# Kernel optimization log

Hardware: AMD Instinct MI355X
Metric: run time of the kernel (lower is better)

Reference implementation:

```python
import jax, jax.numpy as jnp
import numpy as np

N = 100000
E = 1600000
IN_C, HID, HEADS, OUT_C = 128, 32, 4, 32
NEG_SLOPE = 0.2


def gat_layer(x, edge_index, W, att_src, att_dst, bias, concat):
    """PyG-style GATConv: h = xW, per-edge attention, segment softmax over dst, scatter-add."""
    n = x.shape[0]
    H, C = att_src.shape
    h = (x @ W).reshape(n, H, C)                      # [N, H, C]
    src, dst = edge_index[0], edge_index[1]
    a_s = jnp.sum(h * att_src, axis=-1)               # [N, H]
    a_d = jnp.sum(h * att_dst, axis=-1)               # [N, H]
    e = jax.nn.leaky_relu(a_s[src] + a_d[dst], NEG_SLOPE)   # [E, H]
    # numerically stable segment softmax over incoming edges of each dst node
    m = jax.ops.segment_max(e, dst, num_segments=n)   # [N, H]
    ex = jnp.exp(e - m[dst])
    denom = jax.ops.segment_sum(ex, dst, num_segments=n)
    alpha = ex / denom[dst]                           # [E, H]
    msg = h[src] * alpha[:, :, None]                  # [E, H, C]
    out = jax.ops.segment_sum(msg, dst, num_segments=n)  # [N, H, C]
    out = out.reshape(n, H * C) if concat else out.mean(axis=1)
    return out + bias


def add_self_loops(edge_index, n):
    ar = jnp.arange(n, dtype=edge_index.dtype)
    loops = jnp.stack([ar, ar])
    return jnp.concatenate([edge_index, loops], axis=1)


def setup_inputs() -> dict:
    key = jax.random.key(0)
    ks = jax.random.split(key, 10)
    x = jax.random.normal(ks[0], (N, IN_C), dtype=jnp.float32)
    edge_index = jax.random.randint(ks[1], (2, E), 0, N, dtype=jnp.int64)
    s = 0.1
    W1 = jax.random.normal(ks[2], (IN_C, HEADS * HID), dtype=jnp.float32) * s
    att_src1 = jax.random.normal(ks[3], (HEADS, HID), dtype=jnp.float32) * s
    att_dst1 = jax.random.normal(ks[4], (HEADS, HID), dtype=jnp.float32) * s
    b1 = jnp.zeros((HEADS * HID,), dtype=jnp.float32)
    W2 = jax.random.normal(ks[5], (HEADS * HID, OUT_C), dtype=jnp.float32) * s
    att_src2 = jax.random.normal(ks[6], (1, OUT_C), dtype=jnp.float32) * s
    att_dst2 = jax.random.normal(ks[7], (1, OUT_C), dtype=jnp.float32) * s
    b2 = jnp.zeros((OUT_C,), dtype=jnp.float32)
    return {"x": x, "edge_index": edge_index,
            "W1": W1, "att_src1": att_src1, "att_dst1": att_dst1, "b1": b1,
            "W2": W2, "att_src2": att_src2, "att_dst2": att_dst2, "b2": b2}


def reference(x, edge_index, W1, att_src1, att_dst1, b1, W2, att_src2, att_dst2, b2):
    ei = add_self_loops(edge_index, x.shape[0])
    h = gat_layer(x, ei, W1, att_src1, att_dst1, b1, concat=True)
    h = jax.nn.elu(h)
    h = gat_layer(h, ei, W2, att_src2, att_dst2, b2, concat=False)
    return jax.nn.log_softmax(h, axis=1)
```

## Files before the change

### kernel.cpp

```cpp
#include <hip/hip_runtime.h>
#include <hip/hip_fp16.h>
#include <math.h>

#define IN_C   128
#define HEADS  4
#define F1     128
#define OUT_C  32
#define NEG    0.2f
#define SH     8
#define CHA    8192
#define SCB    4096

__device__ __forceinline__ unsigned short f2h(float f) {
    return __half_as_ushort(__float2half_rn(f));
}
__device__ __forceinline__ float h2f(unsigned short u) {
    return __half2float(__ushort_as_half(u));
}
__device__ __forceinline__ float hlo(unsigned u) { return h2f((unsigned short)(u & 0xffffu)); }
__device__ __forceinline__ float hhi(unsigned u) { return h2f((unsigned short)(u >> 16)); }
__device__ __forceinline__ unsigned pk2(float a, float b) {
    return (unsigned)f2h(a) | ((unsigned)f2h(b) << 16);
}
typedef _Float16 h2v __attribute__((ext_vector_type(2)));
__device__ __forceinline__ h2v u2h2(unsigned u) {
    h2v r; __builtin_memcpy(&r, &u, 4); return r;
}
__device__ __forceinline__ float dot2(unsigned a, unsigned b, float c) {
    return __builtin_amdgcn_fdot2(u2h2(a), u2h2(b), c, false);
}
#define PERM_LO 0x05040100u
#define PERM_HI 0x07060302u
__device__ __forceinline__ float pdot(unsigned b, unsigned a, unsigned sel, h2v pv, float c) {
    return __builtin_amdgcn_fdot2(u2h2(__builtin_amdgcn_perm(b, a, sel)), pv, c, false);
}

__global__ __launch_bounds__(256) void k_bhist(
    const int* __restrict__ ei, int* __restrict__ bmat, int E_, int n, int NB, int NC)
{
    __shared__ int h[512];
    int t = threadIdx.x, c = blockIdx.x;
    for (int i = t; i < NB; i += 256) h[i] = 0;
    __syncthreads();
    int e0 = c * CHA, e1 = min(e0 + CHA, E_ + n);
    for (int e = e0 + t; e < e1; e += 256) {
        int d = (e < E_) ? ei[E_ + e] : e - E_;
        atomicAdd(&h[d >> SH], 1);
    }
    __syncthreads();
    for (int i = t; i < NB; i += 256) bmat[i * NC + c] = h[i];
}

__global__ __launch_bounds__(256) void k_scanA(
    int* __restrict__ bmat, int* __restrict__ bsums, int M)
{
    __shared__ int sm[256];
    int t = threadIdx.x;
    int base = blockIdx.x * SCB + t * 16;
    int v[16];
    int s = 0;
    #pragma unroll
    for (int j = 0; j < 16; ++j) {
        int i = base + j;
        v[j] = (i < M) ? bmat[i] : 0;
        s += v[j];
    }
    sm[t] = s;
    __syncthreads();
    for (int off = 1; off < 256; off <<= 1) {
        int a = (t >= off) ? sm[t - off] : 0;
        __syncthreads();
        sm[t] += a;
        __syncthreads();
    }
    int excl = sm[t] - s;
    #pragma unroll
    for (int j = 0; j < 16; ++j) {
        int i = base + j;
        if (i < M) bmat[i] = excl;
        excl += v[j];
    }
    if (t == 255) bsums[blockIdx.x] = sm[255];
}

__global__ __launch_bounds__(256) void k_scanB(int* __restrict__ bsums, int NBLK)
{
    __shared__ int sm[256];
    int t = threadIdx.x;
    int v = (t < NBLK) ? bsums[t] : 0;
    sm[t] = v;
    __syncthreads();
    for (int off = 1; off < 256; off <<= 1) {
        int a = (t >= off) ? sm[t - off] : 0;
        __syncthreads();
        sm[t] += a;
        __syncthreads();
    }
    if (t < NBLK) bsums[t] = sm[t] - v;
}


__global__ __launch_bounds__(256) void k_bscatter(
    const int* __restrict__ ei, const int* __restrict__ bmat,
    const int* __restrict__ bsums, unsigned* __restrict__ recs,
    int E_, int n, int NB, int NC)
{
    __shared__ int cur[512];
    int t = threadIdx.x, c = blockIdx.x;
    for (int i = t; i < NB; i += 256) {
        int m = i * NC + c;
        cur[i] = bmat[m] + bsums[m >> 12];
    }
    __syncthreads();
    int e0 = c * CHA, e1 = min(e0 + CHA, E_ + n);
    for (int e = e0 + t; e < e1; e += 256) {
        int s, d;
        if (e < E_) { s = ei[e]; d = ei[E_ + e]; } else { s = d = e - E_; }
        int b = d >> SH;
        int p = atomicAdd(&cur[b], 1);
        recs[p] = ((unsigned)(d & ((1 << SH) - 1)) << 17) | (unsigned)s;
    }
}

__global__ __launch_bounds__(256) void k_bfill(
    const unsigned* __restrict__ recs, const int* __restrict__ bmat,
    const int* __restrict__ bsums, int* __restrict__ row_off,
    int* __restrict__ csr, int n, int NB, int NC, int EE)
{
    __shared__ int deg[256];
    __shared__ int cur[256];
    int t = threadIdx.x, b = blockIdx.x;
    int m0 = b * NC;
    int r0 = bmat[m0] + bsums[m0 >> 12];
    int r1 = EE;
    if (b + 1 < NB) {
        int m1 = (b + 1) * NC;
        r1 = bmat[m1] + bsums[m1 >> 12];
    }
    deg[t] = 0;
    __syncthreads();
    for (int i = r0 + t; i < r1; i += 256)
        atomicAdd(&deg[recs[i] >> 17], 1);
    __syncthreads();
    int v = deg[t];
    for (int off = 1; off < 256; off <<= 1) {
        int a = (t >= off) ? deg[t - off] : 0;
        __syncthreads();
        deg[t] += a;
        __syncthreads();
    }
    int excl = deg[t] - v;
    int dst = (b << SH) + t;
    if (dst < n) row_off[dst] = r0 + excl;
    cur[t] = excl;
    if (b == NB - 1 && t == 0) row_off[n] = EE;
    __syncthreads();
    for (int i = r0 + t; i < r1; i += 256) {
        unsigned rec = recs[i];
        int dl = rec >> 17;
        int p = atomicAdd(&cur[dl], 1);
        csr[r0 + p] = (int)(rec & 0x1FFFFu);
    }
}

__global__ __launch_bounds__(256) void k_gemm1(
    const float* __restrict__ x, const float* __restrict__ W,
    const float* __restrict__ as_w, const float* __restrict__ ad_w,
    unsigned short* __restrict__ h1h, float* __restrict__ as1,
    float* __restrict__ ad1, int n)
{
    __shared__ unsigned Ws2[64 * 64];
    __shared__ unsigned xs2[64 * 64];
    int t = threadIdx.x;
    int half = blockIdx.x & 1;
    int n0 = (blockIdx.x >> 1) * 64;

    for (int i = t; i < 64 * 16; i += 256) {
        int k2 = i >> 4, c4 = (i & 15) * 4;
        const float* w0 = &W[(2 * k2) * 128 + half * 64 + c4];
        const float* w1 = &W[(2 * k2 + 1) * 128 + half * 64 + c4];
        float4 a = *(const float4*)w0;
        float4 b = *(const float4*)w1;
        uint4 p;
        p.x = pk2(a.x, b.x); p.y = pk2(a.y, b.y);
        p.z = pk2(a.z, b.z); p.w = pk2(a.w, b.w);
        *(uint4*)&Ws2[k2 * 64 + c4] = p;
    }
    for (int i = t; i < 64 * 32; i += 256) {
        int nl = i & 63, k4 = (i >> 6) * 4;
        int nn = n0 + nl;
        float4 v = (nn < n) ? *(const float4*)&x[(size_t)nn * 128 + k4]
                            : make_float4(0.f, 0.f, 0.f, 0.f);
        xs2[(k4 >> 1) * 64 + nl]       = pk2(v.x, v.y);
        xs2[((k4 >> 1) + 1) * 64 + nl] = pk2(v.z, v.w);
    }
    __syncthreads();

    int tx = t & 15, ty = t >> 4;
    float acc[4][4] = {};
    #pragma unroll 4
    for (int k2 = 0; k2 < 64; ++k2) {
        uint4 a = *(uint4*)&xs2[k2 * 64 + ty * 4];
        uint4 b = *(uint4*)&Ws2[k2 * 64 + tx * 4];
        unsigned av[4] = {a.x, a.y, a.z, a.w};
        unsigned bv[4] = {b.x, b.y, b.z, b.w};
        #pragma unroll
        for (int i = 0; i < 4; ++i)
            #pragma unroll
            for (int j = 0; j < 4; ++j)
                acc[i][j] = dot2(av[i], bv[j], acc[i][j]);
    }
    int cbase = half * 64 + tx * 4;
    float4 aws = *(const float4*)&as_w[cbase];
    float4 awd = *(const float4*)&ad_w[cbase];
    float sa[4], sd[4];
    #pragma unroll
    for (int i = 0; i < 4; ++i) {
        int nn = n0 + ty * 4 + i;
        sa[i] = acc[i][0]*aws.x + acc[i][1]*aws.y + acc[i][2]*aws.z + acc[i][3]*aws.w;
        sd[i] = acc[i][0]*awd.x + acc[i][1]*awd.y + acc[i][2]*awd.z + acc[i][3]*awd.w;
        if (nn < n) {
            ushort4 p;
            p.x = f2h(acc[i][0]); p.y = f2h(acc[i][1]);
            p.z = f2h(acc[i][2]); p.w = f2h(acc[i][3]);
            *(ushort4*)&h1h[(size_t)nn * 128 + cbase] = p;
        }
    }
    #pragma unroll
    for (int o = 1; o < 8; o <<= 1) {
        #pragma unroll
        for (int i = 0; i < 4; ++i) {
            sa[i] += __shfl_xor(sa[i], o);
            sd[i] += __shfl_xor(sd[i], o);
        }
    }
    if ((tx & 7) == 0) {
        int head = half * 2 + (tx >> 3);
        #pragma unroll
        for (int i = 0; i < 4; ++i) {
            int nn = n0 + ty * 4 + i;
            if (nn < n) {
                as1[(size_t)nn * 4 + head] = sa[i];
                ad1[(size_t)nn * 4 + head] = sd[i];
            }
        }
    }
}

__global__ __launch_bounds__(256) void k_gat1(
    const int* __restrict__ row_off, const int* __restrict__ csr,
    const float* __restrict__ as1, const float* __restrict__ ad1,
    const unsigned short* __restrict__ h1h, const float* __restrict__ b1,
    const float* __restrict__ W2, const float* __restrict__ as2w,
    const float* __restrict__ ad2w, unsigned short* __restrict__ h2h,
    float* __restrict__ as2, float* __restrict__ ad2, int n)
{
    __shared__ int      s_src[16][36];
    __shared__ unsigned s_pw[16][4][17];
    __shared__ unsigned W2s[64 * 32];
    __shared__ unsigned zs[16][66];
    int t = threadIdx.x;

    for (int i = t; i < 64 * 8; i += 256) {
        int k2 = i >> 3, c4 = (i & 7) * 4;
        float4 a = *(const float4*)&W2[(2 * k2) * 32 + c4];
        float4 b = *(const float4*)&W2[(2 * k2 + 1) * 32 + c4];
        uint4 p;
        p.x = pk2(a.x, b.x); p.y = pk2(a.y, b.y);
        p.z = pk2(a.z, b.z); p.w = pk2(a.w, b.w);
        *(uint4*)&W2s[k2 * 32 + c4] = p;
    }
    __syncthreads();

    int nb = t >> 4;
    int hl = t & 15;
    int node = blockIdx.x * 16 + nb;
    if (node < n) {
        int* ssrc = s_src[nb];
        unsigned (*spw)[17] = s_pw[nb];

        const char* h1b = (const char*)h1h;
        int chb  = hl << 4;
        int head = hl >> 2;

        float4 addv = *(const float4*)&ad1[(size_t)node * 4];
        int beg = row_off[node], end = row_off[node + 1];

        float sr0 = 0.f, sr1 = 0.f, sr2 = 0.f, sr3 = 0.f;
        float acc0 = 0.f, acc1 = 0.f, acc2 = 0.f, acc3 = 0.f;
        float acc4 = 0.f, acc5 = 0.f, acc6 = 0.f, acc7 = 0.f;

        for (int c = beg; c < end; c += 32) {
            int cnt = min(32, end - c);
            int e0 = hl << 1;
            float ls0 = 0.f, ls1 = 0.f, ls2 = 0.f, ls3 = 0.f;
            if (e0 < cnt) {
                int sA = csr[c + e0];
                ssrc[e0] = sA << 8;
                float4 avA = *(const float4*)(as1 + ((unsigned)sA << 2));
                float v;
                unsigned short qa0, qa1, qa2, qa3;
                unsigned short qb0 = 0, qb1 = 0, qb2 = 0, qb3 = 0;
                v = avA.x + addv.x; v = v > 0.f ? v : NEG * v; qa0 = f2h(__expf(fminf(v, 10.f)));
                v = avA.y + addv.y; v = v > 0.f ? v : NEG * v; qa1 = f2h(__expf(fminf(v, 10.f)));
                v = avA.z + addv.z; v = v > 0.f ? v : NEG * v; qa2 = f2h(__expf(fminf(v, 10.f)));
                v = avA.w + addv.w; v = v > 0.f ? v : NEG * v; qa3 = f2h(__expf(fminf(v, 10.f)));
                if (e0 + 1 < cnt) {
                    int sB = csr[c + e0 + 1];
                    ssrc[e0 + 1] = sB << 8;
                    float4 avB = *(const float4*)(as1 + ((unsigned)sB << 2));
                    v = avB.x + addv.x; v = v > 0.f ? v : NEG * v; qb0 = f2h(__expf(fminf(v, 10.f)));
                    v = avB.y + addv.y; v = v > 0.f ? v : NEG * v; qb1 = f2h(__expf(fminf(v, 10.f)));
                    v = avB.z + addv.z; v = v > 0.f ? v : NEG * v; qb2 = f2h(__expf(fminf(v, 10.f)));
                    v = avB.w + addv.w; v = v > 0.f ? v : NEG * v; qb3 = f2h(__expf(fminf(v, 10.f)));
                }
                spw[0][hl] = (unsigned)qa0 | ((unsigned)qb0 << 16);
                spw[1][hl] = (unsigned)qa1 | ((unsigned)qb1 << 16);
                spw[2][hl] = (unsigned)qa2 | ((unsigned)qb2 << 16);
                spw[3][hl] = (unsigned)qa3 | ((unsigned)qb3 << 16);
                ls0 = h2f(qa0) + h2f(qb0);
                ls1 = h2f(qa1) + h2f(qb1);
                ls2 = h2f(qa2) + h2f(qb2);
                ls3 = h2f(qa3) + h2f(qb3);
            }
            #pragma unroll
            for (int o = 8; o; o >>= 1) {
                ls0 += __shfl_xor(ls0, o);
                ls1 += __shfl_xor(ls1, o);
                ls2 += __shfl_xor(ls2, o);
                ls3 += __shfl_xor(ls3, o);
            }
            sr0 += ls0; sr1 += ls1; sr2 += ls2; sr3 += ls3;
            __threadfence_block();

            #define MAC8(A, B, pw) {                                          \
                h2v pv = u2h2(pw);                                            \
                acc0 = pdot(B.x, A.x, PERM_LO, pv, acc0);                     \
                acc1 = pdot(B.x, A.x, PERM_HI, pv, acc1);                     \
                acc2 = pdot(B.y, A.y, PERM_LO, pv, acc2);                     \
// ... 51 lines not shown
        }
        float srh = head == 0 ? sr0 : head == 1 ? sr1 : head == 2 ? sr2 : sr3;
        float inv = 1.0f / srh;
        float4 bb0 = *(const float4*)&b1[hl * 8];
        float4 bb1 = *(const float4*)&b1[hl * 8 + 4];
        float v0 = acc0 * inv + bb0.x;
        float v1 = acc1 * inv + bb0.y;
        float v2 = acc2 * inv + bb0.z;
        float v3 = acc3 * inv + bb0.w;
        float v4 = acc4 * inv + bb1.x;
        float v5 = acc5 * inv + bb1.y;
        float v6 = acc6 * inv + bb1.z;
        float v7 = acc7 * inv + bb1.w;
        v0 = v0 > 0.f ? v0 : (__expf(v0) - 1.f);
        v1 = v1 > 0.f ? v1 : (__expf(v1) - 1.f);
        v2 = v2 > 0.f ? v2 : (__expf(v2) - 1.f);
        v3 = v3 > 0.f ? v3 : (__expf(v3) - 1.f);
        v4 = v4 > 0.f ? v4 : (__expf(v4) - 1.f);
        v5 = v5 > 0.f ? v5 : (__expf(v5) - 1.f);
        v6 = v6 > 0.f ? v6 : (__expf(v6) - 1.f);
        v7 = v7 > 0.f ? v7 : (__expf(v7) - 1.f);

        unsigned* zrow = zs[nb];
        zrow[hl * 4 + 0] = pk2(v0, v1);
        zrow[hl * 4 + 1] = pk2(v2, v3);
        zrow[hl * 4 + 2] = pk2(v4, v5);
        zrow[hl * 4 + 3] = pk2(v6, v7);
        __threadfence_block();
        int c0 = hl * 2;
        float a0 = 0.f, a1 = 0.f;
        #pragma unroll 8
        for (int k2 = 0; k2 < 64; ++k2) {
            unsigned zp = zrow[k2];
            uint2 wp = *(const uint2*)&W2s[k2 * 32 + c0];
            a0 = dot2(zp, wp.x, a0);
            a1 = dot2(zp, wp.y, a1);
        }
        *(unsigned*)&h2h[(size_t)node * 32 + c0] = pk2(a0, a1);
        float2 asw = *(const float2*)&as2w[c0];
        float2 adw = *(const float2*)&ad2w[c0];
        float sa = a0 * asw.x + a1 * asw.y;
        float sd = a0 * adw.x + a1 * adw.y;
        #pragma unroll
        for (int o = 8; o; o >>= 1) {
            sa += __shfl_xor(sa, o);
            sd += __shfl_xor(sd, o);
        }
        if (hl == 0) { as2[node] = sa; ad2[node] = sd; }
    }
}

__global__ __launch_bounds__(256) void k_gat2(
    const int* __restrict__ row_off, const int* __restrict__ csr,
    const float* __restrict__ as2, const float* __restrict__ ad2,
    const unsigned short* __restrict__ h2h, const float* __restrict__ b2,
    float* __restrict__ y, int n)
{
    int nb = threadIdx.x >> 2;
    int hl = threadIdx.x & 3;
    int node = blockIdx.x * 64 + nb;
    if (node >= n) return;
    __shared__ int            s_src[64][34];
    __shared__ unsigned short s_p16[64][34];
    int* ssrc = s_src[nb];
    unsigned short* sp16 = s_p16[nb];

    const char* h2b = (const char*)h2h;
    int chb = hl << 4;

    float addv = ad2[node];
    int beg = row_off[node], end = row_off[node + 1];
    float sr = 0.f;
    float acc0 = 0.f, acc1 = 0.f, acc2 = 0.f, acc3 = 0.f;
    float acc4 = 0.f, acc5 = 0.f, acc6 = 0.f, acc7 = 0.f;

    for (int c = beg; c < end; c += 32) {
        int cnt = min(32, end - c);
        int e0 = hl << 3;
        float ls = 0.f;
        #pragma unroll
        for (int k = 0; k < 8; k += 2) {
            int e = e0 + k;
            if (e < cnt) {
                unsigned short qa, qb = 0;
                int sA = csr[c + e];
                ssrc[e] = sA << 6;
                float v = as2[(unsigned)sA] + addv;
                v = v > 0.f ? v : NEG * v;
                qa = f2h(__expf(fminf(v, 10.f)));
                if (e + 1 < cnt) {
                    int sB = csr[c + e + 1];
                    ssrc[e + 1] = sB << 6;
                    float w2 = as2[(unsigned)sB] + addv;
                    w2 = w2 > 0.f ? w2 : NEG * w2;
                    qb = f2h(__expf(fminf(w2, 10.f)));
                }
                *(unsigned*)&sp16[e] = (unsigned)qa | ((unsigned)qb << 16);
                ls += h2f(qa) + h2f(qb);
            }
        }
        ls += __shfl_xor(ls, 1);
        ls += __shfl_xor(ls, 2);
        sr += ls;
        __threadfence_block();

        #define PAIR2(j) {                                                    \
            int2 oo = *(const int2*)&ssrc[j];                                 \
            unsigned pp = *(const unsigned*)&sp16[j];                         \
            uint4 A = *(const uint4*)(h2b + (unsigned)(oo.x + chb));          \
            uint4 B = *(const uint4*)(h2b + (unsigned)(oo.y + chb));          \
            h2v pv = u2h2(pp);                                                \
            acc0 = pdot(B.x, A.x, PERM_LO, pv, acc0);                         \
            acc1 = pdot(B.x, A.x, PERM_HI, pv, acc1);                         \
            acc2 = pdot(B.y, A.y, PERM_LO, pv, acc2);                         \
            acc3 = pdot(B.y, A.y, PERM_HI, pv, acc3);                         \
            acc4 = pdot(B.z, A.z, PERM_LO, pv, acc4);                         \
            acc5 = pdot(B.z, A.z, PERM_HI, pv, acc5);                         \
            acc6 = pdot(B.w, A.w, PERM_LO, pv, acc6);                         \
            acc7 = pdot(B.w, A.w, PERM_HI, pv, acc7);                         \
        }
        int jj = 0;
        for (; jj + 4 <= cnt; jj += 4) {
            PAIR2(jj);
            PAIR2(jj + 2);
        }
        if (jj + 2 <= cnt) {
            PAIR2(jj);
            jj += 2;
        }
        if (jj < cnt) {
            int o0 = ssrc[jj];
            float p = h2f(sp16[jj]);
            uint4 A = *(const uint4*)(h2b + (unsigned)(o0 + chb));
            acc0 = fmaf(p, hlo(A.x), acc0);
            acc1 = fmaf(p, hhi(A.x), acc1);
            acc2 = fmaf(p, hlo(A.y), acc2);
            acc3 = fmaf(p, hhi(A.y), acc3);
            acc4 = fmaf(p, hlo(A.z), acc4);
            acc5 = fmaf(p, hhi(A.z), acc5);
            acc6 = fmaf(p, hlo(A.w), acc6);
            acc7 = fmaf(p, hhi(A.w), acc7);
        }
        #undef PAIR2
    }
    float inv = 1.0f / sr;
    float4 bb0 = *(const float4*)&b2[hl * 8];
    float4 bb1 = *(const float4*)&b2[hl * 8 + 4];
    float v0 = acc0 * inv + bb0.x;
    float v1 = acc1 * inv + bb0.y;
    float v2 = acc2 * inv + bb0.z;
    float v3 = acc3 * inv + bb0.w;
    float v4 = acc4 * inv + bb1.x;
    float v5 = acc5 * inv + bb1.y;
    float v6 = acc6 * inv + bb1.z;
    float v7 = acc7 * inv + bb1.w;
    float m = fmaxf(fmaxf(fmaxf(v0, v1), fmaxf(v2, v3)),
                    fmaxf(fmaxf(v4, v5), fmaxf(v6, v7)));
    m = fmaxf(m, __shfl_xor(m, 1));
    m = fmaxf(m, __shfl_xor(m, 2));
    float ss = __expf(v0 - m) + __expf(v1 - m) + __expf(v2 - m) + __expf(v3 - m)
             + __expf(v4 - m) + __expf(v5 - m) + __expf(v6 - m) + __expf(v7 - m);
    ss += __shfl_xor(ss, 1);
    ss += __shfl_xor(ss, 2);
    float lg = m + logf(ss);
    float* yr = &y[(size_t)node * OUT_C + hl * 8];
    *(float4*)yr       = make_float4(v0 - lg, v1 - lg, v2 - lg, v3 - lg);
    *(float4*)(yr + 4) = make_float4(v4 - lg, v5 - lg, v6 - lg, v7 - lg);
}

extern "C" void kernel_launch(void* const* d_in, const int* in_sizes, int n_in,
                              void* d_out, int out_size, void* d_ws, size_t ws_size,
                              hipStream_t stream) {
    const float* x    = (const float*)d_in[0];
    const int*   ei   = (const int*)d_in[1];
    const float* W1   = (const float*)d_in[2];
    const float* as1w = (const float*)d_in[3];
    const float* ad1w = (const float*)d_in[4];
    const float* b1   = (const float*)d_in[5];
    const float* W2   = (const float*)d_in[6];
    const float* as2w = (const float*)d_in[7];
    const float* ad2w = (const float*)d_in[8];
    const float* b2   = (const float*)d_in[9];
    float* out = (float*)d_out;

    int n  = in_sizes[0] / IN_C;
    int E_ = in_sizes[1] / 2;
    int EE = E_ + n;

    int NB = (n + (1 << SH) - 1) >> SH;
    int NC = (EE + CHA - 1) / CHA;
    int M  = NB * NC;
    int NBLK = (M + SCB - 1) / SCB;

    char* w = (char*)d_ws;
    size_t off = 0;
    auto take = [&](size_t elems) { void* p = w + off; off += ((elems * 4 + 255) & ~(size_t)255); return p; };
    int* bmat      = (int*)take((size_t)M);
    int* bsums     = (int*)take(256);
    unsigned* recs = (unsigned*)take((size_t)EE);
    int* row_off   = (int*)take((size_t)n + 1);
    int* csr       = (int*)take((size_t)EE);
    float* as1     = (float*)take((size_t)n * 4);
    float* ad1     = (float*)take((size_t)n * 4);
    unsigned short* h1h = (unsigned short*)take((size_t)n * 64);
    unsigned short* h2h = (unsigned short*)take((size_t)n * 16);
    float* as2     = (float*)take((size_t)n);
    float* ad2     = (float*)take((size_t)n);

    k_bhist   <<<NC, 256, 0, stream>>>(ei, bmat, E_, n, NB, NC);
    k_scanA   <<<NBLK, 256, 0, stream>>>(bmat, bsums, M);
    k_scanB   <<<1, 256, 0, stream>>>(bsums, NBLK);
    k_bscatter<<<NC, 256, 0, stream>>>(ei, bmat, bsums, recs, E_, n, NB, NC);
    k_bfill   <<<NB, 256, 0, stream>>>(recs, bmat, bsums, row_off, csr, n, NB, NC, EE);

    int nt = (n + 63) / 64;
    k_gemm1<<<nt * 2, 256, 0, stream>>>(x, W1, as1w, ad1w, h1h, as1, ad1, n);

    int gG = (n + 15) / 16;
    k_gat1<<<gG, 256, 0, stream>>>(row_off, csr, as1, ad1, h1h, b1,
                                   W2, as2w, ad2w, h2h, as2, ad2, n);

    int gG2 = (n + 63) / 64;
    k_gat2<<<gG2, 256, 0, stream>>>(row_off, csr, as2, ad2, h2h, b2, out, n);
}
```

Measured before the change: 302.2 us.

## Fuse histogram into MFMA-based layer-1 GEMM and fold block-sum scan into consumers

Replaces the dot2-based layer-1 GEMM with an MFMA 16x16x32 f16 kernel. It uses swizzled LDS tiles and one block per 64 nodes covering all 128 columns, and adds an LDS-transposed coalesced store of h1. The destination-bucket histogram blocks are merged into the same launch as extra blocks, so the two independent jobs run concurrently. The single-block scanB kernel is removed, and each consumer recomputes the tiny bsums prefix with a warp scan. This cuts kernel launches and speeds up the GEMM. In exchange, every block reserves 48KB of LDS, which may lower occupancy for the histogram blocks, and the write-back relies on a block-level fence rather than a barrier.

Measured after the change: 300.4 us. About the same (-0.6%).

```diff
diff --git a/kernel.cpp b/kernel.cpp
--- a/kernel.cpp
+++ b/kernel.cpp
@@ -22,7 +22,10 @@
 __device__ __forceinline__ unsigned pk2(float a, float b) {
     return (unsigned)f2h(a) | ((unsigned)f2h(b) << 16);
 }
-typedef _Float16 h2v __attribute__((ext_vector_type(2)));
+typedef _Float16 h2v  __attribute__((ext_vector_type(2)));
+typedef _Float16 f16x4v __attribute__((ext_vector_type(4)));
+typedef _Float16 f16x8v __attribute__((ext_vector_type(8)));
+typedef float    f32x4v __attribute__((ext_vector_type(4)));
 __device__ __forceinline__ h2v u2h2(unsigned u) {
     h2v r; __builtin_memcpy(&r, &u, 4); return r;
 }
@@ -35,20 +38,121 @@
     return __builtin_amdgcn_fdot2(u2h2(__builtin_amdgcn_perm(b, a, sel)), pv, c, false);
 }
 
-__global__ __launch_bounds__(256) void k_bhist(
-    const int* __restrict__ ei, int* __restrict__ bmat, int E_, int n, int NB, int NC)
+__global__ __launch_bounds__(256) void k_gemm1h(
+    const float* __restrict__ x, const float* __restrict__ W,
+    const float* __restrict__ as_w, const float* __restrict__ ad_w,
+    const int* __restrict__ ei, int* __restrict__ bmat,
+    unsigned short* __restrict__ h1h, float* __restrict__ as1,
+    float* __restrict__ ad1, int n, int E_, int NB, int NC)
 {
-    __shared__ int h[512];
-    int t = threadIdx.x, c = blockIdx.x;
-    for (int i = t; i < NB; i += 256) h[i] = 0;
-    __syncthreads();
-    int e0 = c * CHA, e1 = min(e0 + CHA, E_ + n);
-    for (int e = e0 + t; e < e1; e += 256) {
-        int d = (e < E_) ? ei[E_ + e] : e - E_;
-        atomicAdd(&h[d >> SH], 1);
-    }
-    __syncthreads();
-    for (int i = t; i < NB; i += 256) bmat[i * NC + c] = h[i];
+    __shared__ char lds[49152];
+    int t = threadIdx.x;
+
+    if ((int)blockIdx.x < NC) {
+        int* h = (int*)lds;
+        int c = blockIdx.x;
+        for (int i = t; i < NB; i += 256) h[i] = 0;
+        __syncthreads();
+        int e0 = c * CHA, e1 = min(e0 + CHA, E_ + n);
+        for (int e = e0 + t; e < e1; e += 256) {
+            int d = (e < E_) ? ei[E_ + e] : e - E_;
+            atomicAdd(&h[d >> SH], 1);
+        }
+        __syncthreads();
+        for (int i = t; i < NB; i += 256) bmat[i * NC + c] = h[i];
+        return;
+    }
+
+    char* xhB = lds;
+    char* wtB = lds + 16384;
+    int n0 = ((int)blockIdx.x - NC) * 64;
+
+    for (int i = t; i < 128 * 32; i += 256) {
+        int k = i >> 5, c4 = (i & 31) * 4;
+        float4 wv = *(const float4*)&W[k * 128 + c4];
+        float vv[4] = {wv.x, wv.y, wv.z, wv.w};
+        #pragma unroll
+        for (int j = 0; j < 4; ++j) {
+            int cc = c4 + j;
+            *(_Float16*)(wtB + cc * 256 + ((2 * k) ^ ((cc & 7) << 4))) = (_Float16)vv[j];
+        }
+    }
+    for (int i = t; i < 64 * 32; i += 256) {
+        int node = i >> 5, k4 = (i & 31) * 4;
+        int nn = n0 + node;
+        float4 v = (nn < n) ? *(const float4*)&x[(size_t)nn * 128 + k4]
+                            : make_float4(0.f, 0.f, 0.f, 0.f);
+        f16x4v hv = { (_Float16)v.x, (_Float16)v.y, (_Float16)v.z, (_Float16)v.w };
+        *(f16x4v*)(xhB + node * 256 + ((2 * k4) ^ ((node & 7) << 4))) = hv;
+    }
+    __syncthreads();
+
+    int w = t >> 6, l = t & 63, g = l >> 4, cl = l & 15;
+    int arow = w * 16 + cl;
+    f32x4v acc[8] = {};
+    #pragma unroll
+    for (int s = 0; s < 4; ++s) {
+        int k2 = 2 * (s * 32 + g * 8);
+        f16x8v a = *(f16x8v*)(xhB + arow * 256 + (k2 ^ ((arow & 7) << 4)));
+        #pragma unroll
+        for (int tt = 0; tt < 8; ++tt) {
+            int col = tt * 16 + cl;
+            f16x8v b = *(f16x8v*)(wtB + col * 256 + (k2 ^ ((col & 7) << 4)));
+            acc[tt] = __builtin_amdgcn_mfma_f32_16x16x32_f16(a, b, acc[tt], 0, 0, 0);
+        }
+    }
+
+    #pragma unroll
+    for (int h = 0; h < 4; ++h) {
+        float asw0 = as_w[h * 32 + cl],      adw0 = ad_w[h * 32 + cl];
+        float asw1 = as_w[h * 32 + 16 + cl], adw1 = ad_w[h * 32 + 16 + cl];
+        float ps[4], pd[4];
+        #pragma unroll
+        for (int r = 0; r < 4; ++r) {
+            ps[r] = acc[2 * h][r] * asw0 + acc[2 * h + 1][r] * asw1;
+            pd[r] = acc[2 * h][r] * adw0 + acc[2 * h + 1][r] * adw1;
+        }
+        #pragma unroll
+        for (int o = 1; o < 16; o <<= 1) {
+            #pragma unroll
+            for (int r = 0; r < 4; ++r) {
+                ps[r] += __shfl_xor(ps[r], o);
+                pd[r] += __shfl_xor(pd[r], o);
+            }
+        }
+        if (cl == h) {
+            #pragma unroll
+            for (int r = 0; r < 4; ++r) {
+                int node = n0 + w * 16 + g * 4 + r;
+                if (node < n) {
+                    as1[(size_t)node * 4 + h] = ps[r];
+                    ad1[(size_t)node * 4 + h] = pd[r];
+                }
+            }
+        }
+    }
+
+    #pragma unroll
+    for (int tt = 0; tt < 8; ++tt) {
+        int cc = tt * 16 + cl;
+        #pragma unroll
+        for (int r = 0; r < 4; ++r) {
+            int rl = w * 16 + g * 4 + r;
+            *(_Float16*)(xhB + rl * 256 + ((2 * cc) ^ ((rl & 7) << 4))) = (_Float16)acc[tt][r];
+        }
+    }
+    __threadfence_block();
+    int rl = w * 16 + cl;
+    int node = n0 + rl;
+    if (node < n) {
+        #pragma unroll
+        for (int i = 0; i < 4; ++i) {
+            int slot = g * 4 + i;
+            uint4 val = *(uint4*)(xhB + rl * 256 + slot * 16);
+            int c0 = 8 * (slot ^ (rl & 7));
+            *(uint4*)&h1h[(size_t)node * 128 + c0] = val;
+        }
+    }
 }
 
 __global__ __launch_bounds__(256) void k_scanA(
@@ -83,33 +187,29 @@
     if (t == 255) bsums[blockIdx.x] = sm[255];
 }
 
-__global__ __launch_bounds__(256) void k_scanB(int* __restrict__ bsums, int NBLK)
-{
-    __shared__ int sm[256];
-    int t = threadIdx.x;
-    int v = (t < NBLK) ? bsums[t] : 0;
-    sm[t] = v;
-    __syncthreads();
-    for (int off = 1; off < 256; off <<= 1) {
-        int a = (t >= off) ? sm[t - off] : 0;
-        __syncthreads();
-        sm[t] += a;
-        __syncthreads();
-    }
-    if (t < NBLK) bsums[t] = sm[t] - v;
-}
-
 
 __global__ __launch_bounds__(256) void k_bscatter(
     const int* __restrict__ ei, const int* __restrict__ bmat,
     const int* __restrict__ bsums, unsigned* __restrict__ recs,
-    int E_, int n, int NB, int NC)
+    int E_, int n, int NB, int NC, int NBLK)
 {
     __shared__ int cur[512];
+    __shared__ int pref[32];
     int t = threadIdx.x, c = blockIdx.x;
+    if (t < 32) {
+        int v0 = (t < NBLK) ? bsums[t] : 0;
+        int v = v0;
+        #pragma unroll
+        for (int o = 1; o < 32; o <<= 1) {
+            int u = __shfl_up(v, o);
+            if (t >= o) v += u;
+        }
+        pref[t] = v - v0;
+    }
+    __syncthreads();
     for (int i = t; i < NB; i += 256) {
         int m = i * NC + c;
-        cur[i] = bmat[m] + bsums[m >> 12];
+        cur[i] = bmat[m] + pref[m >> 12];
     }
     __syncthreads();
     int e0 = c * CHA, e1 = min(e0 + CHA, E_ + n);
@@ -125,20 +225,31 @@
 __global__ __launch_bounds__(256) void k_bfill(
     const unsigned* __restrict__ recs, const int* __restrict__ bmat,
     const int* __restrict__ bsums, int* __restrict__ row_off,
-    int* __restrict__ csr, int n, int NB, int NC, int EE)
+    int* __restrict__ csr, int n, int NB, int NC, int EE, int NBLK)
 {
     __shared__ int deg[256];
     __shared__ int cur[256];
+    __shared__ int pref[32];
     int t = threadIdx.x, b = blockIdx.x;
+    if (t < 32) {
+        int v0 = (t < NBLK) ? bsums[t] : 0;
+        int v = v0;
+        #pragma unroll
+        for (int o = 1; o < 32; o <<= 1) {
+            int u = __shfl_up(v, o);
+            if (t >= o) v += u;
+        }
+        pref[t] = v - v0;
+    }
+    deg[t] = 0;
+    __syncthreads();
     int m0 = b * NC;
-    int r0 = bmat[m0] + bsums[m0 >> 12];
+    int r0 = bmat[m0] + pref[m0 >> 12];
     int r1 = EE;
     if (b + 1 < NB) {
         int m1 = (b + 1) * NC;
-        r1 = bmat[m1] + bsums[m1 >> 12];
-    }
-    deg[t] = 0;
-    __syncthreads();
+        r1 = bmat[m1] + pref[m1 >> 12];
+    }
     for (int i = r0 + t; i < r1; i += 256)
         atomicAdd(&deg[recs[i] >> 17], 1);
     __syncthreads();
@@ -160,90 +271,6 @@
         int dl = rec >> 17;
         int p = atomicAdd(&cur[dl], 1);
         csr[r0 + p] = (int)(rec & 0x1FFFFu);
-    }
-}
-
-__global__ __launch_bounds__(256) void k_gemm1(
-    const float* __restrict__ x, const float* __restrict__ W,
-    const float* __restrict__ as_w, const float* __restrict__ ad_w,
-    unsigned short* __restrict__ h1h, float* __restrict__ as1,
-    float* __restrict__ ad1, int n)
-{
-    __shared__ unsigned Ws2[64 * 64];
-    __shared__ unsigned xs2[64 * 64];
-    int t = threadIdx.x;
-    int half = blockIdx.x & 1;
-    int n0 = (blockIdx.x >> 1) * 64;
-
-    for (int i = t; i < 64 * 16; i += 256) {
-        int k2 = i >> 4, c4 = (i & 15) * 4;
-        const float* w0 = &W[(2 * k2) * 128 + half * 64 + c4];
-        const float* w1 = &W[(2 * k2 + 1) * 128 + half * 64 + c4];
-        float4 a = *(const float4*)w0;
-        float4 b = *(const float4*)w1;
-        uint4 p;
-        p.x = pk2(a.x, b.x); p.y = pk2(a.y, b.y);
-        p.z = pk2(a.z, b.z); p.w = pk2(a.w, b.w);
-        *(uint4*)&Ws2[k2 * 64 + c4] = p;
-    }
-    for (int i = t; i < 64 * 32; i += 256) {
-        int nl = i & 63, k4 = (i >> 6) * 4;
-        int nn = n0 + nl;
-        float4 v = (nn < n) ? *(const float4*)&x[(size_t)nn * 128 + k4]
-                            : make_float4(0.f, 0.f, 0.f, 0.f);
-        xs2[(k4 >> 1) * 64 + nl]       = pk2(v.x, v.y);
-        xs2[((k4 >> 1) + 1) * 64 + nl] = pk2(v.z, v.w);
-    }
-    __syncthreads();
-
-    int tx = t & 15, ty = t >> 4;
-    float acc[4][4] = {};
-    #pragma unroll 4
-    for (int k2 = 0; k2 < 64; ++k2) {
-        uint4 a = *(uint4*)&xs2[k2 * 64 + ty * 4];
-        uint4 b = *(uint4*)&Ws2[k2 * 64 + tx * 4];
-        unsigned av[4] = {a.x, a.y, a.z, a.w};
-        unsigned bv[4] = {b.x, b.y, b.z, b.w};
-        #pragma unroll
-        for (int i = 0; i < 4; ++i)
-            #pragma unroll
-            for (int j = 0; j < 4; ++j)
-                acc[i][j] = dot2(av[i], bv[j], acc[i][j]);
-    }
-    int cbase = half * 64 + tx * 4;
-    float4 aws = *(const float4*)&as_w[cbase];
-    float4 awd = *(const float4*)&ad_w[cbase];
-    float sa[4], sd[4];
-    #pragma unroll
-    for (int i = 0; i < 4; ++i) {
-        int nn = n0 + ty * 4 + i;
-        sa[i] = acc[i][0]*aws.x + acc[i][1]*aws.y + acc[i][2]*aws.z + acc[i][3]*aws.w;
-        sd[i] = acc[i][0]*awd.x + acc[i][1]*awd.y + acc[i][2]*awd.z + acc[i][3]*awd.w;
-        if (nn < n) {
-            ushort4 p;
-            p.x = f2h(acc[i][0]); p.y = f2h(acc[i][1]);
-            p.z = f2h(acc[i][2]); p.w = f2h(acc[i][3]);
-            *(ushort4*)&h1h[(size_t)nn * 128 + cbase] = p;
-        }
-    }
-    #pragma unroll
-    for (int o = 1; o < 8; o <<= 1) {
-        #pragma unroll
-        for (int i = 0; i < 4; ++i) {
-            sa[i] += __shfl_xor(sa[i], o);
-            sd[i] += __shfl_xor(sd[i], o);
-        }
-    }
-    if ((tx & 7) == 0) {
-        int head = half * 2 + (tx >> 3);
-        #pragma unroll
-        for (int i = 0; i < 4; ++i) {
-            int nn = n0 + ty * 4 + i;
-            if (nn < n) {
-                as1[(size_t)nn * 4 + head] = sa[i];
-                ad1[(size_t)nn * 4 + head] = sd[i];
-            }
-        }
     }
 }
 
@@ -597,14 +624,13 @@
     float* as2     = (float*)take((size_t)n);
     float* ad2     = (float*)take((size_t)n);
 
-    k_bhist   <<<NC, 256, 0, stream>>>(ei, bmat, E_, n, NB, NC);
+    int nt64 = (n + 63) / 64;
+    k_gemm1h<<<NC + nt64, 256, 0, stream>>>(x, W1, as1w, ad1w, ei, bmat,
+                                            h1h, as1, ad1, n, E_, NB, NC);
+
     k_scanA   <<<NBLK, 256, 0, stream>>>(bmat, bsums, M);
-    k_scanB   <<<1, 256, 0, stream>>>(bsums, NBLK);
-    k_bscatter<<<NC, 256, 0, stream>>>(ei, bmat, bsums, recs, E_, n, NB, NC);
-    k_bfill   <<<NB, 256, 0, stream>>>(recs, bmat, bsums, row_off, csr, n, NB, NC, EE);
-
-    int nt = (n + 63) / 64;
-    k_gemm1<<<nt * 2, 256, 0, stream>>>(x, W1, as1w, ad1w, h1h, as1, ad1, n);
+    k_bscatter<<<NC, 256, 0, stream>>>(ei, bmat, bsums, recs, E_, n, NB, NC, NBLK);
+    k_bfill   <<<NB, 256, 0, stream>>>(recs, bmat, bsums, row_off, csr, n, NB, NC, EE, NBLK);
 
     int gG = (n + 15) / 16;
     k_gat1<<<gG, 256, 0, stream>>>(row_off, csr, as1, ad1, h1h, b1,
```

## Replace bucketed CSR build with global-atomic degree count, scan, and fill

Applied to the files above, without the earlier changes.

Drops the two-level bucket histogram, scatter and per-bucket fill in favor of counting per-node in-degrees with global atomics, then one block-local scan and an atomic-cursor fill of the CSR array. The degree count is fused into the first GEMM launch as extra blocks, and the scan of block sums is folded into the consumer kernels, each of which recomputes a small prefix in shared memory. This removes several launches and the intermediate records array, at the cost of heavily contended global atomics on random destinations and a nondeterministic edge order within each row.

Result: slower. 440.0 us (+45.6%).

```diff
diff --git a/kernel.cpp b/kernel.cpp
--- a/kernel.cpp
+++ b/kernel.cpp
@@ -7,7 +7,6 @@
 #define F1     128
 #define OUT_C  32
 #define NEG    0.2f
-#define SH     8
 #define CHA    8192
 #define SCB    4096
 
@@ -35,145 +34,30 @@
     return __builtin_amdgcn_fdot2(u2h2(__builtin_amdgcn_perm(b, a, sel)), pv, c, false);
 }
 
-__global__ __launch_bounds__(256) void k_bhist(
-    const int* __restrict__ ei, int* __restrict__ bmat, int E_, int n, int NB, int NC)
-{
-    __shared__ int h[512];
-    int t = threadIdx.x, c = blockIdx.x;
-    for (int i = t; i < NB; i += 256) h[i] = 0;
-    __syncthreads();
-    int e0 = c * CHA, e1 = min(e0 + CHA, E_ + n);
-    for (int e = e0 + t; e < e1; e += 256) {
-        int d = (e < E_) ? ei[E_ + e] : e - E_;
-        atomicAdd(&h[d >> SH], 1);
-    }
-    __syncthreads();
-    for (int i = t; i < NB; i += 256) bmat[i * NC + c] = h[i];
-}
-
-__global__ __launch_bounds__(256) void k_scanA(
-    int* __restrict__ bmat, int* __restrict__ bsums, int M)
-{
-    __shared__ int sm[256];
-    int t = threadIdx.x;
-    int base = blockIdx.x * SCB + t * 16;
-    int v[16];
-    int s = 0;
-    #pragma unroll
-    for (int j = 0; j < 16; ++j) {
-        int i = base + j;
-        v[j] = (i < M) ? bmat[i] : 0;
-        s += v[j];
-    }
-    sm[t] = s;
-    __syncthreads();
-    for (int off = 1; off < 256; off <<= 1) {
-        int a = (t >= off) ? sm[t - off] : 0;
-        __syncthreads();
-        sm[t] += a;
-        __syncthreads();
-    }
-    int excl = sm[t] - s;
-    #pragma unroll
-    for (int j = 0; j < 16; ++j) {
-        int i = base + j;
-        if (i < M) bmat[i] = excl;
-        excl += v[j];
-    }
-    if (t == 255) bsums[blockIdx.x] = sm[255];
-}
-
-__global__ __launch_bounds__(256) void k_scanB(int* __restrict__ bsums, int NBLK)
-{
-    __shared__ int sm[256];
-    int t = threadIdx.x;
-    int v = (t < NBLK) ? bsums[t] : 0;
-    sm[t] = v;
-    __syncthreads();
-    for (int off = 1; off < 256; off <<= 1) {
-        int a = (t >= off) ? sm[t - off] : 0;
-        __syncthreads();
-        sm[t] += a;
-        __syncthreads();
-    }
-    if (t < NBLK) bsums[t] = sm[t] - v;
-}
-
-
-__global__ __launch_bounds__(256) void k_bscatter(
-    const int* __restrict__ ei, const int* __restrict__ bmat,
-    const int* __restrict__ bsums, unsigned* __restrict__ recs,
-    int E_, int n, int NB, int NC)
-{
-    __shared__ int cur[512];
-    int t = threadIdx.x, c = blockIdx.x;
-    for (int i = t; i < NB; i += 256) {
-        int m = i * NC + c;
-        cur[i] = bmat[m] + bsums[m >> 12];
-    }
-    __syncthreads();
-    int e0 = c * CHA, e1 = min(e0 + CHA, E_ + n);
-    for (int e = e0 + t; e < e1; e += 256) {
-        int s, d;
-        if (e < E_) { s = ei[e]; d = ei[E_ + e]; } else { s = d = e - E_; }
-        int b = d >> SH;
-        int p = atomicAdd(&cur[b], 1);
-        recs[p] = ((unsigned)(d & ((1 << SH) - 1)) << 17) | (unsigned)s;
-    }
-}
-
-__global__ __launch_bounds__(256) void k_bfill(
-    const unsigned* __restrict__ recs, const int* __restrict__ bmat,
-    const int* __restrict__ bsums, int* __restrict__ row_off,
-    int* __restrict__ csr, int n, int NB, int NC, int EE)
-{
-    __shared__ int deg[256];
-    __shared__ int cur[256];
-    int t = threadIdx.x, b = blockIdx.x;
-    int m0 = b * NC;
-    int r0 = bmat[m0] + bsums[m0 >> 12];
-    int r1 = EE;
-    if (b + 1 < NB) {
-        int m1 = (b + 1) * NC;
-        r1 = bmat[m1] + bsums[m1 >> 12];
-    }
-    deg[t] = 0;
-    __syncthreads();
-    for (int i = r0 + t; i < r1; i += 256)
-        atomicAdd(&deg[recs[i] >> 17], 1);
-    __syncthreads();
-    int v = deg[t];
-    for (int off = 1; off < 256; off <<= 1) {
-        int a = (t >= off) ? deg[t - off] : 0;
-        __syncthreads();
-        deg[t] += a;
-        __syncthreads();
-    }
-    int excl = deg[t] - v;
-    int dst = (b << SH) + t;
-    if (dst < n) row_off[dst] = r0 + excl;
-    cur[t] = excl;
-    if (b == NB - 1 && t == 0) row_off[n] = EE;
-    __syncthreads();
-    for (int i = r0 + t; i < r1; i += 256) {
-        unsigned rec = recs[i];
-        int dl = rec >> 17;
-        int p = atomicAdd(&cur[dl], 1);
-        csr[r0 + p] = (int)(rec & 0x1FFFFu);
-    }
-}
-
-__global__ __launch_bounds__(256) void k_gemm1(
+__global__ __launch_bounds__(256) void k_gemm1c(
     const float* __restrict__ x, const float* __restrict__ W,
     const float* __restrict__ as_w, const float* __restrict__ ad_w,
+    const int* __restrict__ ei, int* __restrict__ deg,
     unsigned short* __restrict__ h1h, float* __restrict__ as1,
-    float* __restrict__ ad1, int n)
+    float* __restrict__ ad1, int n, int E_, int NC)
 {
     __shared__ unsigned Ws2[64 * 64];
     __shared__ unsigned xs2[64 * 64];
     int t = threadIdx.x;
-    int half = blockIdx.x & 1;
-    int n0 = (blockIdx.x >> 1) * 64;
+
+    if ((int)blockIdx.x < NC) {
+        int c = blockIdx.x;
+        int e0 = c * CHA, e1 = min(e0 + CHA, E_ + n);
+        for (int e = e0 + t; e < e1; e += 256) {
+            int d = (e < E_) ? ei[E_ + e] : e - E_;
+            atomicAdd(&deg[d], 1);
+        }
+        return;
+    }
+
+    int gb = (int)blockIdx.x - NC;
+    int half = gb & 1;
+    int n0 = (gb >> 1) * 64;
 
     for (int i = t; i < 64 * 16; i += 256) {
         int k2 = i >> 4, c4 = (i & 15) * 4;
@@ -247,20 +131,96 @@
     }
 }
 
+__global__ __launch_bounds__(256) void k_scanA(
+    int* __restrict__ deg, int* __restrict__ row_off,
+    int* __restrict__ bsums, int M)
+{
+    __shared__ int sm[256];
+    int t = threadIdx.x;
+    int base = blockIdx.x * SCB + t * 16;
+    int v[16];
+    int s = 0;
+    #pragma unroll
+    for (int j = 0; j < 16; ++j) {
+        int i = base + j;
+        v[j] = (i < M) ? deg[i] : 0;
+        s += v[j];
+    }
+    sm[t] = s;
+    __syncthreads();
+    for (int off = 1; off < 256; off <<= 1) {
+        int a = (t >= off) ? sm[t - off] : 0;
+        __syncthreads();
+        sm[t] += a;
+        __syncthreads();
+    }
+    int excl = sm[t] - s;
+    #pragma unroll
+    for (int j = 0; j < 16; ++j) {
+        int i = base + j;
+        if (i < M) { deg[i] = excl; row_off[i] = excl; }
+        excl += v[j];
+    }
+    if (t == 255) bsums[blockIdx.x] = sm[255];
+}
+
+__global__ __launch_bounds__(256) void k_fill(
+    const int* __restrict__ ei, int* __restrict__ deg,
+    const int* __restrict__ bsums, int* __restrict__ csr,
+    int E_, int n, int NBLK)
+{
+    __shared__ int pref[32];
+    int t = threadIdx.x;
+    if (t < 32) {
+        int v0 = (t < NBLK) ? bsums[t] : 0;
+        int v = v0;
+        #pragma unroll
+        for (int o = 1; o < 32; o <<= 1) {
+            int u = __shfl_up(v, o);
+            if (t >= o) v += u;
+        }
+        pref[t] = v - v0;
+    }
+    __syncthreads();
+    int base = blockIdx.x * 2048;
+    #pragma unroll
+    for (int k = 0; k < 8; ++k) {
+        int e = base + k * 256 + t;
+        if (e < E_ + n) {
+            int s, d;
+            if (e < E_) { s = ei[e]; d = ei[E_ + e]; } else { s = d = e - E_; }
+            int p = atomicAdd(&deg[d], 1) + pref[d >> 12];
+            csr[p] = s;
+        }
+    }
+}
+
 __global__ __launch_bounds__(256) void k_gat1(
     const int* __restrict__ row_off, const int* __restrict__ csr,
+    const int* __restrict__ bsums,
     const float* __restrict__ as1, const float* __restrict__ ad1,
     const unsigned short* __restrict__ h1h, const float* __restrict__ b1,
     const float* __restrict__ W2, const float* __restrict__ as2w,
     const float* __restrict__ ad2w, unsigned short* __restrict__ h2h,
-    float* __restrict__ as2, float* __restrict__ ad2, int n)
+    float* __restrict__ as2, float* __restrict__ ad2, int n, int EE, int NBLK)
 {
     __shared__ int      s_src[16][36];
     __shared__ unsigned s_pw[16][4][17];
     __shared__ unsigned W2s[64 * 32];
     __shared__ unsigned zs[16][66];
+    __shared__ int      pref[32];
     int t = threadIdx.x;
 
+    if (t < 32) {
+        int v0 = (t < NBLK) ? bsums[t] : 0;
+        int v = v0;
+        #pragma unroll
+        for (int o = 1; o < 32; o <<= 1) {
+            int u = __shfl_up(v, o);
+            if (t >= o) v += u;
+        }
+        pref[t] = v - v0;
+    }
     for (int i = t; i < 64 * 8; i += 256) {
         int k2 = i >> 3, c4 = (i & 7) * 4;
         float4 a = *(const float4*)&W2[(2 * k2) * 32 + c4];
@@ -284,7 +244,8 @@
         int head = hl >> 2;
 
         float4 addv = *(const float4*)&ad1[(size_t)node * 4];
-        int beg = row_off[node], end = row_off[node + 1];
+        int beg = row_off[node] + pref[node >> 12];
+        int end = (node + 1 < n) ? row_off[node + 1] + pref[(node + 1) >> 12] : EE;
 
         float sr0 = 0.f, sr1 = 0.f, sr2 = 0.f, sr3 = 0.f;
         float acc0 = 0.f, acc1 = 0.f, acc2 = 0.f, acc3 = 0.f;
@@ -442,120 +403,137 @@
 
 __global__ __launch_bounds__(256) void k_gat2(
     const int* __restrict__ row_off, const int* __restrict__ csr,
+    const int* __restrict__ bsums,
     const float* __restrict__ as2, const float* __restrict__ ad2,
     const unsigned short* __restrict__ h2h, const float* __restrict__ b2,
-    float* __restrict__ y, int n)
+    float* __restrict__ y, int n, int EE, int NBLK)
 {
-    int nb = threadIdx.x >> 2;
-    int hl = threadIdx.x & 3;
-    int node = blockIdx.x * 64 + nb;
-    if (node >= n) return;
     __shared__ int            s_src[64][34];
     __shared__ unsigned short s_p16[64][34];
-    int* ssrc = s_src[nb];
-    unsigned short* sp16 = s_p16[nb];
-
-    const char* h2b = (const char*)h2h;
-    int chb = hl << 4;
-
-    float addv = ad2[node];
-    int beg = row_off[node], end = row_off[node + 1];
-    float sr = 0.f;
-    float acc0 = 0.f, acc1 = 0.f, acc2 = 0.f, acc3 = 0.f;
-    float acc4 = 0.f, acc5 = 0.f, acc6 = 0.f, acc7 = 0.f;
-
-    for (int c = beg; c < end; c += 32) {
-        int cnt = min(32, end - c);
-        int e0 = hl << 3;
-        float ls = 0.f;
-        #pragma unroll
-        for (int k = 0; k < 8; k += 2) {
-            int e = e0 + k;
-            if (e < cnt) {
-                unsigned short qa, qb = 0;
-                int sA = csr[c + e];
-                ssrc[e] = sA << 6;
-                float v = as2[(unsigned)sA] + addv;
-                v = v > 0.f ? v : NEG * v;
-                qa = f2h(__expf(fminf(v, 10.f)));
-                if (e + 1 < cnt) {
-                    int sB = csr[c + e + 1];
-                    ssrc[e + 1] = sB << 6;
-                    float w2 = as2[(unsigned)sB] + addv;
-                    w2 = w2 > 0.f ? w2 : NEG * w2;
-                    qb = f2h(__expf(fminf(w2, 10.f)));
+    __shared__ int            pref[32];
+    int t = threadIdx.x;
+    if (t < 32) {
+        int v0 = (t < NBLK) ? bsums[t] : 0;
+        int v = v0;
+        #pragma unroll
+        for (int o = 1; o < 32; o <<= 1) {
+            int u = __shfl_up(v, o);
+            if (t >= o) v += u;
+        }
+        pref[t] = v - v0;
+    }
+    __syncthreads();
+
+    int nb = t >> 2;
+    int hl = t & 3;
+    int node = blockIdx.x * 64 + nb;
+    if (node < n) {
+        int* ssrc = s_src[nb];
+        unsigned short* sp16 = s_p16[nb];
+
+        const char* h2b = (const char*)h2h;
+        int chb = hl << 4;
+
+        float addv = ad2[node];
+        int beg = row_off[node] + pref[node >> 12];
+        int end = (node + 1 < n) ? row_off[node + 1] + pref[(node + 1) >> 12] : EE;
+        float sr = 0.f;
+        float acc0 = 0.f, acc1 = 0.f, acc2 = 0.f, acc3 = 0.f;
+        float acc4 = 0.f, acc5 = 0.f, acc6 = 0.f, acc7 = 0.f;
+
+        for (int c = beg; c < end; c += 32) {
+            int cnt = min(32, end - c);
+            int e0 = hl << 3;
+            float ls = 0.f;
+            #pragma unroll
+            for (int k = 0; k < 8; k += 2) {
+                int e = e0 + k;
+                if (e < cnt) {
+                    unsigned short qa, qb = 0;
+                    int sA = csr[c + e];
+                    ssrc[e] = sA << 6;
+                    float v = as2[(unsigned)sA] + addv;
+                    v = v > 0.f ? v : NEG * v;
+                    qa = f2h(__expf(fminf(v, 10.f)));
+                    if (e + 1 < cnt) {
+                        int sB = csr[c + e + 1];
+                        ssrc[e + 1] = sB << 6;
+                        float w2 = as2[(unsigned)sB] + addv;
+                        w2 = w2 > 0.f ? w2 : NEG * w2;
+                        qb = f2h(__expf(fminf(w2, 10.f)));
+                    }
+                    *(unsigned*)&sp16[e] = (unsigned)qa | ((unsigned)qb << 16);
+                    ls += h2f(qa) + h2f(qb);
                 }
-                *(unsigned*)&sp16[e] = (unsigned)qa | ((unsigned)qb << 16);
-                ls += h2f(qa) + h2f(qb);
-            }
-        }
-        ls += __shfl_xor(ls, 1);
-        ls += __shfl_xor(ls, 2);
-        sr += ls;
-        __threadfence_block();
-
-        #define PAIR2(j) {                                                    \
-            int2 oo = *(const int2*)&ssrc[j];                                 \
-            unsigned pp = *(const unsigned*)&sp16[j];                         \
-            uint4 A = *(const uint4*)(h2b + (unsigned)(oo.x + chb));          \
-            uint4 B = *(const uint4*)(h2b + (unsigned)(oo.y + chb));          \
-            h2v pv = u2h2(pp);                                                \
-            acc0 = pdot(B.x, A.x, PERM_LO, pv, acc0);                         \
-            acc1 = pdot(B.x, A.x, PERM_HI, pv, acc1);                         \
-            acc2 = pdot(B.y, A.y, PERM_LO, pv, acc2);                         \
-            acc3 = pdot(B.y, A.y, PERM_HI, pv, acc3);                         \
-            acc4 = pdot(B.z, A.z, PERM_LO, pv, acc4);                         \
-            acc5 = pdot(B.z, A.z, PERM_HI, pv, acc5);                         \
-            acc6 = pdot(B.w, A.w, PERM_LO, pv, acc6);                         \
-            acc7 = pdot(B.w, A.w, PERM_HI, pv, acc7);                         \
-        }
-        int jj = 0;
-        for (; jj + 4 <= cnt; jj += 4) {
-            PAIR2(jj);
-            PAIR2(jj + 2);
-        }
-        if (jj + 2 <= cnt) {
-            PAIR2(jj);
-            jj += 2;
-        }
-        if (jj < cnt) {
-            int o0 = ssrc[jj];
-            float p = h2f(sp16[jj]);
-            uint4 A = *(const uint4*)(h2b + (unsigned)(o0 + chb));
-            acc0 = fmaf(p, hlo(A.x), acc0);
-            acc1 = fmaf(p, hhi(A.x), acc1);
-            acc2 = fmaf(p, hlo(A.y), acc2);
-            acc3 = fmaf(p, hhi(A.y), acc3);
-            acc4 = fmaf(p, hlo(A.z), acc4);
-            acc5 = fmaf(p, hhi(A.z), acc5);
-            acc6 = fmaf(p, hlo(A.w), acc6);
-            acc7 = fmaf(p, hhi(A.w), acc7);
-        }
-        #undef PAIR2
-    }
-    float inv = 1.0f / sr;
-    float4 bb0 = *(const float4*)&b2[hl * 8];
-    float4 bb1 = *(const float4*)&b2[hl * 8 + 4];
-    float v0 = acc0 * inv + bb0.x;
-    float v1 = acc1 * inv + bb0.y;
-    float v2 = acc2 * inv + bb0.z;
-    float v3 = acc3 * inv + bb0.w;
-    float v4 = acc4 * inv + bb1.x;
-    float v5 = acc5 * inv + bb1.y;
-    float v6 = acc6 * inv + bb1.z;
-    float v7 = acc7 * inv + bb1.w;
-    float m = fmaxf(fmaxf(fmaxf(v0, v1), fmaxf(v2, v3)),
-                    fmaxf(fmaxf(v4, v5), fmaxf(v6, v7)));
-    m = fmaxf(m, __shfl_xor(m, 1));
-    m = fmaxf(m, __shfl_xor(m, 2));
-    float ss = __expf(v0 - m) + __expf(v1 - m) + __expf(v2 - m) + __expf(v3 - m)
-             + __expf(v4 - m) + __expf(v5 - m) + __expf(v6 - m) + __expf(v7 - m);
-    ss += __shfl_xor(ss, 1);
-    ss += __shfl_xor(ss, 2);
-    float lg = m + logf(ss);
-    float* yr = &y[(size_t)node * OUT_C + hl * 8];
-    *(float4*)yr       = make_float4(v0 - lg, v1 - lg, v2 - lg, v3 - lg);
-    *(float4*)(yr + 4) = make_float4(v4 - lg, v5 - lg, v6 - lg, v7 - lg);
+            }
+            ls += __shfl_xor(ls, 1);
+            ls += __shfl_xor(ls, 2);
+            sr += ls;
+            __threadfence_block();
+
+            #define PAIR2(j) {                                                \
+                int2 oo = *(const int2*)&ssrc[j];                             \
+                unsigned pp = *(const unsigned*)&sp16[j];                     \
+                uint4 A = *(const uint4*)(h2b + (unsigned)(oo.x + chb));      \
+                uint4 B = *(const uint4*)(h2b + (unsigned)(oo.y + chb));      \
+                h2v pv = u2h2(pp);                                            \
+                acc0 = pdot(B.x, A.x, PERM_LO, pv, acc0);                     \
+                acc1 = pdot(B.x, A.x, PERM_HI, pv, acc1);                     \
+                acc2 = pdot(B.y, A.y, PERM_LO, pv, acc2);                     \
+                acc3 = pdot(B.y, A.y, PERM_HI, pv, acc3);                     \
+                acc4 = pdot(B.z, A.z, PERM_LO, pv, acc4);                     \
+                acc5 = pdot(B.z, A.z, PERM_HI, pv, acc5);                     \
+                acc6 = pdot(B.w, A.w, PERM_LO, pv, acc6);                     \
+                acc7 = pdot(B.w, A.w, PERM_HI, pv, acc7);                     \
+            }
+            int jj = 0;
+            for (; jj + 4 <= cnt; jj += 4) {
+                PAIR2(jj);
+                PAIR2(jj + 2);
+            }
+            if (jj + 2 <= cnt) {
+                PAIR2(jj);
+                jj += 2;
+            }
+            if (jj < cnt) {
+                int o0 = ssrc[jj];
+                float p = h2f(sp16[jj]);
+                uint4 A = *(const uint4*)(h2b + (unsigned)(o0 + chb));
+                acc0 = fmaf(p, hlo(A.x), acc0);
+                acc1 = fmaf(p, hhi(A.x), acc1);
+                acc2 = fmaf(p, hlo(A.y), acc2);
+                acc3 = fmaf(p, hhi(A.y), acc3);
+                acc4 = fmaf(p, hlo(A.z), acc4);
+                acc5 = fmaf(p, hhi(A.z), acc5);
+                acc6 = fmaf(p, hlo(A.w), acc6);
+                acc7 = fmaf(p, hhi(A.w), acc7);
+            }
+            #undef PAIR2
+        }
+        float inv = 1.0f / sr;
+        float4 bb0 = *(const float4*)&b2[hl * 8];
+        float4 bb1 = *(const float4*)&b2[hl * 8 + 4];
+        float v0 = acc0 * inv + bb0.x;
+        float v1 = acc1 * inv + bb0.y;
+        float v2 = acc2 * inv + bb0.z;
+        float v3 = acc3 * inv + bb0.w;
+        float v4 = acc4 * inv + bb1.x;
+        float v5 = acc5 * inv + bb1.y;
+        float v6 = acc6 * inv + bb1.z;
+        float v7 = acc7 * inv + bb1.w;
+        float m = fmaxf(fmaxf(fmaxf(v0, v1), fmaxf(v2, v3)),
+                        fmaxf(fmaxf(v4, v5), fmaxf(v6, v7)));
+        m = fmaxf(m, __shfl_xor(m, 1));
+        m = fmaxf(m, __shfl_xor(m, 2));
+        float ss = __expf(v0 - m) + __expf(v1 - m) + __expf(v2 - m) + __expf(v3 - m)
+                 + __expf(v4 - m) + __expf(v5 - m) + __expf(v6 - m) + __expf(v7 - m);
+        ss += __shfl_xor(ss, 1);
+        ss += __shfl_xor(ss, 2);
+        float lg = m + logf(ss);
+        float* yr = &y[(size_t)node * OUT_C + hl * 8];
+        *(float4*)yr       = make_float4(v0 - lg, v1 - lg, v2 - lg, v3 - lg);
+        *(float4*)(yr + 4) = make_float4(v4 - lg, v5 - lg, v6 - lg, v7 - lg);
+    }
 }
 
 extern "C" void kernel_launch(void* const* d_in, const int* in_sizes, int n_in,
@@ -577,18 +555,15 @@
     int E_ = in_sizes[1] / 2;
     int EE = E_ + n;
 
-    int NB = (n + (1 << SH) - 1) >> SH;
-    int NC = (EE + CHA - 1) / CHA;
-    int M  = NB * NC;
-    int NBLK = (M + SCB - 1) / SCB;
+    int NC   = (EE + CHA - 1) / CHA;
+    int NBLK = (n + SCB - 1) / SCB;
 
     char* w = (char*)d_ws;
     size_t off = 0;
     auto take = [&](size_t elems) { void* p = w + off; off += ((elems * 4 + 255) & ~(size_t)255); return p; };
-    int* bmat      = (int*)take((size_t)M);
+    int* deg       = (int*)take((size_t)n);
+    int* row_off   = (int*)take((size_t)n);
     int* bsums     = (int*)take(256);
-    unsigned* recs = (unsigned*)take((size_t)EE);
-    int* row_off   = (int*)take((size_t)n + 1);
     int* csr       = (int*)take((size_t)EE);
     float* as1     = (float*)take((size_t)n * 4);
     float* ad1     = (float*)take((size_t)n * 4);
@@ -597,19 +572,20 @@
     float* as2     = (float*)take((size_t)n);
     float* ad2     = (float*)take((size_t)n);
 
-    k_bhist   <<<NC, 256, 0, stream>>>(ei, bmat, E_, n, NB, NC);
-    k_scanA   <<<NBLK, 256, 0, stream>>>(bmat, bsums, M);
-    k_scanB   <<<1, 256, 0, stream>>>(bsums, NBLK);
-    k_bscatter<<<NC, 256, 0, stream>>>(ei, bmat, bsums, recs, E_, n, NB, NC);
-    k_bfill   <<<NB, 256, 0, stream>>>(recs, bmat, bsums, row_off, csr, n, NB, NC, EE);
-
-    int nt = (n + 63) / 64;
-    k_gemm1<<<nt * 2, 256, 0, stream>>>(x, W1, as1w, ad1w, h1h, as1, ad1, n);
+    hipMemsetAsync(deg, 0, (size_t)n * sizeof(int), stream);
+
+    int nt2 = 2 * ((n + 63) / 64);
+    k_gemm1c<<<NC + nt2, 256, 0, stream>>>(x, W1, as1w, ad1w, ei, deg,
+                                           h1h, as1, ad1, n, E_, NC);
+
+    k_scanA<<<NBLK, 256, 0, stream>>>(deg, row_off, bsums, n);
+    k_fill <<<(EE + 2047) / 2048, 256, 0, stream>>>(ei, deg, bsums, csr, E_, n, NBLK);
 
     int gG = (n + 15) / 16;
-    k_gat1<<<gG, 256, 0, stream>>>(row_off, csr, as1, ad1, h1h, b1,
-                                   W2, as2w, ad2w, h2h, as2, ad2, n);
+    k_gat1<<<gG, 256, 0, stream>>>(row_off, csr, bsums, as1, ad1, h1h, b1,
+                                   W2, as2w, ad2w, h2h, as2, ad2, n, EE, NBLK);
 
     int gG2 = (n + 63) / 64;
-    k_gat2<<<gG2, 256, 0, stream>>>(row_off, csr, as2, ad2, h2h, b2, out, n);
-}
+    k_gat2<<<gG2, 256, 0, stream>>>(row_off, csr, bsums, as2, ad2, h2h, b2,
+                                    out, n, EE, NBLK);
+}
```
